# Optimization experiments

Hardware: AMD Instinct MI355X
Metric: run time of the kernel (lower is better)

The kernel has to match this reference:

```python
import jax, jax.numpy as jnp
import numpy as np

B, S, T = 2, 4096, 4096
SRC, DST, WIDTH = 512, 512, 128
BLK = 128  # JAKAL_ADDITIVE_ROUTE_BLOCK_SIZE default


def setup_inputs() -> dict:
    key = jax.random.key(0)
    ks = jax.random.split(key, 7)
    return {
        "source_val": jax.random.normal(ks[0], (B, S, SRC), jnp.float32),
        "target_val": jax.random.normal(ks[1], (B, T, DST), jnp.float32),
        "Ws": jax.random.normal(ks[2], (WIDTH, SRC), jnp.float32) * 0.02,  # source_proj weight
        "Wt": jax.random.normal(ks[3], (WIDTH, DST), jnp.float32) * 0.02,  # target_proj weight
        "ws_out": jax.random.normal(ks[4], (WIDTH,), jnp.float32) * 0.02,  # source_out weight
        "wt_out": jax.random.normal(ks[5], (WIDTH,), jnp.float32) * 0.02,  # target_out weight
        "w_int": jax.random.normal(ks[6], (WIDTH,), jnp.float32) * 0.02,   # interaction_weight
        "bias": jnp.zeros((), jnp.float32),
    }


def reference(source_val, target_val, Ws, Wt, ws_out, wt_out, w_int, bias):
    # Projections (Linear without bias): y = x @ W.T
    ps = jnp.einsum('bsd,wd->bsw', source_val, Ws)   # [B,S,WIDTH]
    pt = jnp.einsum('btd,wd->btw', target_val, Wt)   # [B,T,WIDTH]
    s_lin = jnp.einsum('bsw,w->bs', ps, ws_out)      # [B,S]
    t_lin = jnp.einsum('btw,w->bt', pt, wt_out)      # [B,T]

    nblk = S // BLK
    # Block the source axis, matching the torch block loop (avoids a [B,S,T,W] tensor).
    ps_blocks = ps.reshape(B, nblk, BLK, WIDTH).transpose(1, 0, 2, 3)   # [nblk,B,BLK,W]
    sl_blocks = s_lin.reshape(B, nblk, BLK).transpose(1, 0, 2)          # [nblk,B,BLK]

    def block_scores(_, xs):
        ps_blk, sl_blk = xs
        # SiLU of the elementwise bilinear interaction, then low-rank weighted reduce.
        inter = jax.nn.silu(ps_blk[:, :, None, :] * pt[:, None, :, :])  # [B,BLK,T,W]
        sc = jnp.einsum('bktw,w->bkt', inter, w_int)
        sc = sc + sl_blk[:, :, None] + t_lin[:, None, :] + bias
        return None, sc

    _, out = jax.lax.scan(block_scores, None, (ps_blocks, sl_blocks))   # [nblk,B,BLK,T]
    return out.transpose(1, 0, 2, 3).reshape(B, S, T)
```

## Files before the change

kernel.cpp:

```cpp
#include <hip/hip_runtime.h>
#include <cstdint>
#include <cstddef>

#define B_ 2
#define S_ 4096
#define T_ 4096
#define D_ 512
#define W_ 128

#define A0C (-0.0006958f)
#define A1C (0.2529946f)
#define A2C (-0.0226345f)
#define A3C (0.0022173f)
#define A4C (-0.00011668f)
#define ZCUT 2.5f
#define ROWCAP 65536

typedef __attribute__((ext_vector_type(8))) short bf16x8;
typedef __attribute__((ext_vector_type(4))) float f32x4;

__device__ __forceinline__ uint16_t f2bf(float f){
  uint32_t u = __float_as_uint(f);
  u += 0x7FFFu + ((u >> 16) & 1u);
  return (uint16_t)(u >> 16);
}
__device__ __forceinline__ float bf2f(uint16_t h){
  return __uint_as_float(((uint32_t)h) << 16);
}

__device__ __forceinline__ void gl_lds16(const void* g, void* l){
  __builtin_amdgcn_global_load_lds(
      (const __attribute__((address_space(1))) void*)g,
      (__attribute__((address_space(3))) void*)l, 16, 0, 0);
}

union F4 { float4 v; float f[4]; };

template<int INBF>
__global__ void prep_k(const void* __restrict__ Ws, const void* __restrict__ Wt,
                       const void* __restrict__ wso, const void* __restrict__ wto,
                       const void* __restrict__ wi, const void* __restrict__ bias,
                       float* __restrict__ WsT, float* __restrict__ WtT,
                       float* __restrict__ wsof, float* __restrict__ wtof,
                       float* __restrict__ wif, float* __restrict__ cbias,
                       int* __restrict__ rowCnt){
  auto cv = [](const void* p, int i)->float{
    if (INBF) return bf2f(((const uint16_t*)p)[i]);
    return ((const float*)p)[i];
  };
  const void* in = (blockIdx.x & 1) ? Wt : Ws;
  float* out = (blockIdx.x & 1) ? WtT : WsT;
  int base = (blockIdx.x >> 1) * 4096;
  for (int o = base + threadIdx.x; o < base + 4096; o += blockDim.x){
    int d = o >> 7, w = o & (W_ - 1);
    out[o] = cv(in, w * D_ + d);
  }
  if (blockIdx.x == 0){
    if (threadIdx.x < W_){
      wsof[threadIdx.x] = cv(wso, threadIdx.x);
      wtof[threadIdx.x] = cv(wto, threadIdx.x);
      wif[threadIdx.x]  = cv(wi,  threadIdx.x);
    }
    __syncthreads();
    if (threadIdx.x == 0){
      float s = 0.f;
      for (int k = 0; k < W_; ++k) s += wif[k];
      cbias[0] = cv(bias, 0) + A0C * s;
      rowCnt[0] = 0;
    }
  }
}

template<int INBF, int MODE>
__global__ __launch_bounds__(256) void proj_k(const void* __restrict__ xraw,
        const float* __restrict__ WT, const float* __restrict__ wout,
        const float* __restrict__ wint,
        float* __restrict__ pT, float* __restrict__ lin,
        uint16_t* __restrict__ feat){
  __shared__ float xl[64 * 36];
  __shared__ float wl[64 * 128];
  int tid = threadIdx.x;
  int tx = tid & 31, ty = tid >> 5;
  int rowBase = blockIdx.x * 32;
  float acc[4][4] = {};
  for (int c = 0; c < 8; ++c){
    int d0 = c * 64;
    const float4* wt4 = (const float4*)(WT + (size_t)d0 * W_);
    float4* wl4 = (float4*)wl;
    #pragma unroll
    for (int p = 0; p < 8; ++p){ int q = tid + 256 * p; wl4[q] = wt4[q]; }
    #pragma unroll
    for (int p = 0; p < 2; ++p){
      int q = tid + 256 * p;
      int r = q >> 4, dq = q & 15;
      float v0, v1, v2, v3;
      if (INBF){
        const uint16_t* xp = (const uint16_t*)xraw + (size_t)(rowBase + r) * D_ + d0 + dq * 4;
        ushort4 u = *(const ushort4*)xp;
        v0 = bf2f(u.x); v1 = bf2f(u.y); v2 = bf2f(u.z); v3 = bf2f(u.w);
      } else {
        const float* xp = (const float*)xraw + (size_t)(rowBase + r) * D_ + d0 + dq * 4;
        float4 u = *(const float4*)xp;
        v0 = u.x; v1 = u.y; v2 = u.z; v3 = u.w;
      }
      xl[(dq*4+0)*36 + r] = v0;
      xl[(dq*4+1)*36 + r] = v1;
      xl[(dq*4+2)*36 + r] = v2;
      xl[(dq*4+3)*36 + r] = v3;
    }
    __syncthreads();
    #pragma unroll 4
    for (int d = 0; d < 64; ++d){
      F4 a, w;
      a.v = *(const float4*)(xl + d * 36 + ty * 4);
      w.v = *(const float4*)(wl + d * 128 + tx * 4);
      #pragma unroll
      for (int i = 0; i < 4; ++i)
        #pragma unroll
        for (int j = 0; j < 4; ++j)
          acc[i][j] = fmaf(a.f[i], w.f[j], acc[i][j]);
    }
    __syncthreads();
  }
  float* tile = wl;
  #pragma unroll
  for (int i = 0; i < 4; ++i)
    #pragma unroll
    for (int j = 0; j < 4; ++j)
      tile[(tx*4 + j) * 33 + ty*4 + i] = acc[i][j];
  F4 wo; wo.v = *(const float4*)(wout + tx * 4);
  F4 wiv;
  if (MODE == 0) wiv.v = *(const float4*)(wint + tx * 4);
  #pragma unroll
  for (int i = 0; i < 4; ++i){
    int r = rowBase + ty * 4 + i;
    float s = acc[i][0]*wo.f[0] + acc[i][1]*wo.f[1] + acc[i][2]*wo.f[2] + acc[i][3]*wo.f[3];
    #pragma unroll
    for (int off = 16; off >= 1; off >>= 1) s += __shfl_xor(s, off, 32);
    if (tx == 0) lin[r] = s;
    ushort4 g[5];
    uint16_t* gp = (uint16_t*)g;
    #pragma unroll
    for (int j = 0; j < 4; ++j){
      float p = acc[i][j];
      float p2 = p*p, p4 = p2*p2, p6 = p4*p2, p8 = p4*p4;
      float e0, e1, e2, e3, e4;
      if (MODE == 0){
        float wq = wiv.f[j];
        e0 = 0.5f * wq * p; e1 = A1C * wq * p2; e2 = A2C * wq * p4;
        e3 = A3C * wq * p6; e4 = A4C * wq * p8;
      } else {
        e0 = p; e1 = p2; e2 = p4; e3 = p6; e4 = p8;
      }
      gp[0*4+j] = f2bf(e0); gp[1*4+j] = f2bf(e1); gp[2*4+j] = f2bf(e2);
      gp[3*4+j] = f2bf(e3); gp[4*4+j] = f2bf(e4);
    }
    uint16_t* o = feat + (size_t)r * 640 + tx * 4;
    *(ushort4*)(o)       = g[0];
    *(ushort4*)(o + 128) = g[1];
    *(ushort4*)(o + 256) = g[2];
    *(ushort4*)(o + 384) = g[3];
    *(ushort4*)(o + 512) = g[4];
  }
  __syncthreads();
  {
    int w = tid >> 1, h = tid & 1;
    int b = rowBase >> 12;
    int sb = rowBase & (S_ - 1);
    float* dst = pT + ((size_t)(b * W_ + w)) * S_ + sb + h * 16;
    const float* src = tile + w * 33 + h * 16;
    #pragma unroll
    for (int k = 0; k < 4; ++k){
      float4 o = make_float4(src[k*4+0], src[k*4+1], src[k*4+2], src[k*4+3]);
      *(float4*)(dst + k * 4) = o;
    }
  }
}

__global__ void maxT_k(const float* __restrict__ ptT, float* __restrict__ maxT){
  int bw = blockIdx.x;
  int tid = threadIdx.x;
  const float* c = ptT + (size_t)bw * T_;
  float m = 0.f;
  for (int t = tid; t < T_; t += 256) m = fmaxf(m, fabsf(c[t]));
  #pragma unroll
  for (int off = 32; off >= 1; off >>= 1) m = fmaxf(m, __shfl_xor(m, off, 64));
  __shared__ float red[4];
  if ((tid & 63) == 0) red[tid >> 6] = m;
  __syncthreads();
  if (tid == 0)
    maxT[bw] = fmaxf(fmaxf(red[0], red[1]), fmaxf(red[2], red[3]));
}

template<int OUTBF>
__global__ __launch_bounds__(256) void gemm_k(const uint16_t* __restrict__ fA,
      const uint16_t* __restrict__ fB, const float* __restrict__ slin,
      const float* __restrict__ tlin, const float* __restrict__ cbias,
      void* __restrict__ outv){
  __shared__ __align__(16) uint16_t As[2][128 * 32];
  __shared__ __align__(16) uint16_t Bs[2][128 * 32];
  int tid = threadIdx.x, lane = tid & 63, wv = tid >> 6;
  int quad = lane >> 4, lr = lane & 15;
  int rowT = blockIdx.y * 128, colT = blockIdx.x * 128;
  int b = rowT >> 12;
  int r0 = lane >> 2, c0 = (lane & 3) * 8;
  int mBase = (wv & 1) * 64, nBase = (wv >> 1) * 64;

  f32x4 acc[4][4];
  #pragma unroll
  for (int i = 0; i < 4; ++i)
    #pragma unroll
    for (int j = 0; j < 4; ++j)
      acc[i][j] = (f32x4){0.f, 0.f, 0.f, 0.f};

  const uint16_t* aBase = fA + (size_t)rowT * 640;
  const uint16_t* bBase = fB + ((size_t)b * T_ + colT) * 640;

  const int NSTEP = 20;
  #pragma unroll
  for (int h = 0; h < 2; ++h){
    int q = 2 * wv + h;
    gl_lds16(aBase + (size_t)(16 * q + r0) * 640 + c0, &As[0][q * 512]);
    gl_lds16(bBase + (size_t)(16 * q + r0) * 640 + c0, &Bs[0][q * 512]);
  }
  for (int step = 0; step < NSTEP; ++step){
    int cur = step & 1;
    if (step + 1 < NSTEP){
      int kc = (step + 1) * 32;
      #pragma unroll
      for (int h = 0; h < 2; ++h){
        int q = 2 * wv + h;
        gl_lds16(aBase + (size_t)(16 * q + r0) * 640 + kc + c0, &As[cur ^ 1][q * 512]);
        gl_lds16(bBase + (size_t)(16 * q + r0) * 640 + kc + c0, &Bs[cur ^ 1][q * 512]);
      }
      asm volatile("s_waitcnt vmcnt(4)" ::: "memory");
    } else {
      asm volatile("s_waitcnt vmcnt(0)" ::: "memory");
    }
    __builtin_amdgcn_s_barrier();
    bf16x8 af[4], bfr[4];
    #pragma unroll
    for (int i = 0; i < 4; ++i)
      af[i] = *(const bf16x8*)&As[cur][(mBase + i * 16 + lr) * 32 + quad * 8];
    #pragma unroll
    for (int j = 0; j < 4; ++j)
      bfr[j] = *(const bf16x8*)&Bs[cur][(nBase + j * 16 + lr) * 32 + quad * 8];
    #pragma unroll
    for (int i = 0; i < 4; ++i)
      #pragma unroll
      for (int j = 0; j < 4; ++j)
        acc[i][j] = __builtin_amdgcn_mfma_f32_16x16x32_bf16(bfr[j], af[i], acc[i][j], 0, 0, 0);
    __builtin_amdgcn_s_barrier();
  }

  float cb = cbias[0];
  #pragma unroll
  for (int i = 0; i < 4; ++i){
    int srow = rowT + mBase + i * 16 + lr;
    float sl = slin[srow] + cb;
    #pragma unroll
    for (int j = 0; j < 4; ++j){
      int t0 = colT + nBase + j * 16 + quad * 4;
      F4 tl; tl.v = *(const float4*)(tlin + b * T_ + t0);
      float o0 = acc[i][j][0] + sl + tl.f[0];
      float o1 = acc[i][j][1] + sl + tl.f[1];
      float o2 = acc[i][j][2] + sl + tl.f[2];
      float o3 = acc[i][j][3] + sl + tl.f[3];
      size_t oi = (size_t)srow * T_ + t0;
      if (OUTBF){
        ushort4 pk = make_ushort4(f2bf(o0), f2bf(o1), f2bf(o2), f2bf(o3));
        *(ushort4*)((uint16_t*)outv + oi) = pk;
      } else {
        *(float4*)((float*)outv + oi) = make_float4(o0, o1, o2, o3);
      }
    }
  }
}

__global__ void flagrows_k(const float* __restrict__ psT, const float* __restrict__ maxT,
                           uint32_t* __restrict__ rowList, int* __restrict__ rowCnt){
  int w = blockIdx.x, b = blockIdx.y;
  int tid = threadIdx.x;
  float mt = maxT[b * W_ + w];
  const float* psc = psT + (size_t)(b * W_ + w) * S_;
  for (int s = tid; s < S_; s += 256){
    float p = psc[s];
    if (fabsf(p) * mt > ZCUT){
      int k = atomicAdd(rowCnt, 1);
      if (k < ROWCAP)
        rowList[k] = ((uint32_t)b << 19) | ((uint32_t)w << 12) | (uint32_t)s;
    }
  }
}

template<int OUTBF>
__global__ __launch_bounds__(256) void fixscan_k(const float* __restrict__ psT,
        const float* __restrict__ ptT, const float* __restrict__ wint,
        const uint16_t* __restrict__ fA, const uint16_t* __restrict__ fB,
        const uint32_t* __restrict__ rowList, const int* __restrict__ rowCnt,
        void* __restrict__ outv){
  int n = *rowCnt; if (n > ROWCAP) n = ROWCAP;
  int tid = threadIdx.x;
  for (int job = blockIdx.x; job < n; job += gridDim.x){
    uint32_t pk = rowList[job];
    int b = (int)(pk >> 19), w = (int)((pk >> 12) & 127u), s = (int)(pk & 4095u);
    float wi = wint[w];
    float p = psT[(size_t)(b * W_ + w) * S_ + s];
    const float* ptc = ptT + (size_t)(b * W_ + w) * T_;
    const uint16_t* fa = fA + ((size_t)b * S_ + s) * 640 + w;
    float a0 = bf2f(fa[0]),   a1 = bf2f(fa[128]), a2 = bf2f(fa[256]);
    float a3 = bf2f(fa[384]), a4 = bf2f(fa[512]);
    for (int t = tid; t < T_; t += 256){
      float q = ptc[t];
      float z = p * q;
      if (fabsf(z) > ZCUT){
        const uint16_t* fb = fB + ((size_t)b * T_ + t) * 640 + w;
        float dot = a0 * bf2f(fb[0]) + a1 * bf2f(fb[128]) + a2 * bf2f(fb[256])
                  + a3 * bf2f(fb[384]) + a4 * bf2f(fb[512]);
        float sil = z / (1.0f + __expf(-z));
        float corr = wi * sil - dot - A0C * wi;
        size_t idx = ((size_t)b * S_ + s) * T_ + t;
        if (OUTBF){
          uint32_t* wp = (uint32_t*)outv + (idx >> 1);
          bool hi = (idx & 1u) != 0;
          uint32_t assumed, old = *wp;
          do {
            assumed = old;
            uint16_t h = hi ? (uint16_t)(assumed >> 16) : (uint16_t)(assumed & 0xFFFFu);
            uint16_t nh = f2bf(bf2f(h) + corr);
            uint32_t nw = hi ? ((assumed & 0x0000FFFFu) | ((uint32_t)nh << 16))
                             : ((assumed & 0xFFFF0000u) | (uint32_t)nh);
            old = atomicCAS(wp, assumed, nw);
          } while (old != assumed);
        } else {
          atomicAdd((float*)outv + idx, corr);
        }
      }
    }
  }
}

extern "C" void kernel_launch(void* const* d_in, const int* in_sizes, int n_in,
                              void* d_out, int out_size, void* d_ws, size_t ws_size,
                              hipStream_t stream){
  char* ws = (char*)d_ws;
  size_t off = 0;
  auto alloc = [&](size_t bytes)->char*{
    char* p = ws + off; off += (bytes + 255) & ~(size_t)255; return p;
  };
  float*    WsT  = (float*)   alloc((size_t)D_*W_*4);
  float*    WtT  = (float*)   alloc((size_t)D_*W_*4);
  float*    wsof = (float*)   alloc(W_*4);
  float*    wtof = (float*)   alloc(W_*4);
  float*    wif  = (float*)   alloc(W_*4);
  float*    cbias= (float*)   alloc(4);
  int*      rowCnt=(int*)     alloc(4);
  uint32_t* rowList=(uint32_t*)alloc((size_t)ROWCAP*4);
  float*    psT  = (float*)   alloc((size_t)B_*S_*W_*4);
  float*    ptT  = (float*)   alloc((size_t)B_*T_*W_*4);
  float*    slin = (float*)   alloc((size_t)B_*S_*4);
  float*    tlin = (float*)   alloc((size_t)B_*T_*4);
  float*    maxT = (float*)   alloc((size_t)B_*W_*4);
  uint16_t* featA= (uint16_t*)alloc((size_t)B_*S_*640*2);
  uint16_t* featB= (uint16_t*)alloc((size_t)B_*T_*640*2);

  bool inbf  = (in_sizes[0] == (int)((size_t)B_*S_*D_*2));
  bool outbf = (out_size    == (int)((size_t)B_*S_*T_*2));

  if (inbf){
    hipLaunchKernelGGL((prep_k<1>), dim3(32), dim3(256), 0, stream,
        d_in[2], d_in[3], d_in[4], d_in[5], d_in[6], d_in[7],
        WsT, WtT, wsof, wtof, wif, cbias, rowCnt);
    hipLaunchKernelGGL((proj_k<1,0>), dim3(B_*S_/32), dim3(256), 0, stream,
        d_in[0], WsT, wsof, wif, psT, slin, featA);
    hipLaunchKernelGGL((proj_k<1,1>), dim3(B_*T_/32), dim3(256), 0, stream,
        d_in[1], WtT, wtof, wif, ptT, tlin, featB);
  } else {
    hipLaunchKernelGGL((prep_k<0>), dim3(32), dim3(256), 0, stream,
        d_in[2], d_in[3], d_in[4], d_in[5], d_in[6], d_in[7],
        WsT, WtT, wsof, wtof, wif, cbias, rowCnt);
    hipLaunchKernelGGL((proj_k<0,0>), dim3(B_*S_/32), dim3(256), 0, stream,
        d_in[0], WsT, wsof, wif, psT, slin, featA);
    hipLaunchKernelGGL((proj_k<0,1>), dim3(B_*T_/32), dim3(256), 0, stream,
        d_in[1], WtT, wtof, wif, ptT, tlin, featB);
  }
  hipLaunchKernelGGL(maxT_k, dim3(B_*W_), dim3(256), 0, stream, ptT, maxT);
  if (outbf)
    hipLaunchKernelGGL((gemm_k<1>), dim3(T_/128, B_*S_/128), dim3(256), 0, stream,
        featA, featB, slin, tlin, cbias, d_out);
  else
    hipLaunchKernelGGL((gemm_k<0>), dim3(T_/128, B_*S_/128), dim3(256), 0, stream,
        featA, featB, slin, tlin, cbias, d_out);
  hipLaunchKernelGGL(flagrows_k, dim3(W_, B_), dim3(256), 0, stream,
      psT, maxT, rowList, rowCnt);
  if (outbf)
    hipLaunchKernelGGL((fixscan_k<1>), dim3(2048), dim3(256), 0, stream,
        psT, ptT, wif, featA, featB, rowList, rowCnt, d_out);
  else
    hipLaunchKernelGGL((fixscan_k<0>), dim3(2048), dim3(256), 0, stream,
        psT, ptT, wif, featA, featB, rowList, rowCnt, d_out);
}
```

Before: 314.9 us.

## Fuse maxT into projection and flag-list into fixup kernel, halve proj tile

Removes the standalone maxT reduction kernel: the target projection now folds per-column absolute maxima into maxT through atomicMax on the float bit pattern, and prep_k zeroes maxT. The row-flagging and fixup kernels are merged into one kernel per (w,b) that builds its flagged-row list in shared memory, which removes a launch, the global row counter and the ROWCAP limit. The projection tile shrinks from 32 to 16 rows per block to double the block count, at the cost of reloading the weight slab more times overall. The merged fixup runs only 256 blocks and processes its rows serially per block, so load imbalance across columns may be worse than the old 2048-block job pool.

```diff
diff --git a/kernel.cpp b/kernel.cpp
--- a/kernel.cpp
+++ b/kernel.cpp
@@ -14,7 +14,6 @@
 #define A3C (0.0022173f)
 #define A4C (-0.00011668f)
 #define ZCUT 2.5f
-#define ROWCAP 65536
 
 typedef __attribute__((ext_vector_type(8))) short bf16x8;
 typedef __attribute__((ext_vector_type(4))) float f32x4;
@@ -43,7 +42,7 @@
                        float* __restrict__ WsT, float* __restrict__ WtT,
                        float* __restrict__ wsof, float* __restrict__ wtof,
                        float* __restrict__ wif, float* __restrict__ cbias,
-                       int* __restrict__ rowCnt){
+                       float* __restrict__ maxT){
   auto cv = [](const void* p, int i)->float{
     if (INBF) return bf2f(((const uint16_t*)p)[i]);
     return ((const float*)p)[i];
@@ -55,6 +54,9 @@
     int d = o >> 7, w = o & (W_ - 1);
     out[o] = cv(in, w * D_ + d);
   }
+  if (blockIdx.x == 1){
+    maxT[threadIdx.x] = 0.f;
+  }
   if (blockIdx.x == 0){
     if (threadIdx.x < W_){
       wsof[threadIdx.x] = cv(wso, threadIdx.x);
@@ -66,7 +68,6 @@
       float s = 0.f;
       for (int k = 0; k < W_; ++k) s += wif[k];
       cbias[0] = cv(bias, 0) + A0C * s;
-      rowCnt[0] = 0;
     }
   }
 }
@@ -76,22 +77,21 @@
         const float* __restrict__ WT, const float* __restrict__ wout,
         const float* __restrict__ wint,
         float* __restrict__ pT, float* __restrict__ lin,
-        uint16_t* __restrict__ feat){
-  __shared__ float xl[64 * 36];
+        uint16_t* __restrict__ feat, float* __restrict__ maxT){
+  __shared__ float xl[64 * 18];
   __shared__ float wl[64 * 128];
   int tid = threadIdx.x;
   int tx = tid & 31, ty = tid >> 5;
-  int rowBase = blockIdx.x * 32;
-  float acc[4][4] = {};
+  int rowBase = blockIdx.x * 16;
+  float acc[2][4] = {};
   for (int c = 0; c < 8; ++c){
     int d0 = c * 64;
     const float4* wt4 = (const float4*)(WT + (size_t)d0 * W_);
     float4* wl4 = (float4*)wl;
     #pragma unroll
     for (int p = 0; p < 8; ++p){ int q = tid + 256 * p; wl4[q] = wt4[q]; }
-    #pragma unroll
-    for (int p = 0; p < 2; ++p){
-      int q = tid + 256 * p;
+    {
+      int q = tid;
       int r = q >> 4, dq = q & 15;
       float v0, v1, v2, v3;
       if (INBF){
@@ -103,37 +103,38 @@
         float4 u = *(const float4*)xp;
         v0 = u.x; v1 = u.y; v2 = u.z; v3 = u.w;
       }
-      xl[(dq*4+0)*36 + r] = v0;
-      xl[(dq*4+1)*36 + r] = v1;
-      xl[(dq*4+2)*36 + r] = v2;
-      xl[(dq*4+3)*36 + r] = v3;
+      xl[(dq*4+0)*18 + r] = v0;
+      xl[(dq*4+1)*18 + r] = v1;
+      xl[(dq*4+2)*18 + r] = v2;
+      xl[(dq*4+3)*18 + r] = v3;
     }
     __syncthreads();
     #pragma unroll 4
     for (int d = 0; d < 64; ++d){
-      F4 a, w;
-      a.v = *(const float4*)(xl + d * 36 + ty * 4);
+      float a0 = xl[d * 18 + ty * 2 + 0];
+      float a1 = xl[d * 18 + ty * 2 + 1];
+      F4 w;
       w.v = *(const float4*)(wl + d * 128 + tx * 4);
       #pragma unroll
-      for (int i = 0; i < 4; ++i)
-        #pragma unroll
-        for (int j = 0; j < 4; ++j)
-          acc[i][j] = fmaf(a.f[i], w.f[j], acc[i][j]);
+      for (int j = 0; j < 4; ++j){
+        acc[0][j] = fmaf(a0, w.f[j], acc[0][j]);
+        acc[1][j] = fmaf(a1, w.f[j], acc[1][j]);
+      }
     }
     __syncthreads();
   }
   float* tile = wl;
   #pragma unroll
-  for (int i = 0; i < 4; ++i)
+  for (int i = 0; i < 2; ++i)
     #pragma unroll
     for (int j = 0; j < 4; ++j)
-      tile[(tx*4 + j) * 33 + ty*4 + i] = acc[i][j];
+      tile[(tx*4 + j) * 17 + ty*2 + i] = acc[i][j];
   F4 wo; wo.v = *(const float4*)(wout + tx * 4);
   F4 wiv;
   if (MODE == 0) wiv.v = *(const float4*)(wint + tx * 4);
   #pragma unroll
-  for (int i = 0; i < 4; ++i){
-    int r = rowBase + ty * 4 + i;
+  for (int i = 0; i < 2; ++i){
+    int r = rowBase + ty * 2 + i;
     float s = acc[i][0]*wo.f[0] + acc[i][1]*wo.f[1] + acc[i][2]*wo.f[2] + acc[i][3]*wo.f[3];
     #pragma unroll
     for (int off = 16; off >= 1; off >>= 1) s += __shfl_xor(s, off, 32);
@@ -163,33 +164,25 @@
     *(ushort4*)(o + 512) = g[4];
   }
   __syncthreads();
+  int b = rowBase >> 12;
   {
     int w = tid >> 1, h = tid & 1;
-    int b = rowBase >> 12;
     int sb = rowBase & (S_ - 1);
-    float* dst = pT + ((size_t)(b * W_ + w)) * S_ + sb + h * 16;
-    const float* src = tile + w * 33 + h * 16;
-    #pragma unroll
-    for (int k = 0; k < 4; ++k){
+    float* dst = pT + ((size_t)(b * W_ + w)) * S_ + sb + h * 8;
+    const float* src = tile + w * 17 + h * 8;
+    #pragma unroll
+    for (int k = 0; k < 2; ++k){
       float4 o = make_float4(src[k*4+0], src[k*4+1], src[k*4+2], src[k*4+3]);
       *(float4*)(dst + k * 4) = o;
     }
   }
-}
-
-__global__ void maxT_k(const float* __restrict__ ptT, float* __restrict__ maxT){
-  int bw = blockIdx.x;
-  int tid = threadIdx.x;
-  const float* c = ptT + (size_t)bw * T_;
-  float m = 0.f;
-  for (int t = tid; t < T_; t += 256) m = fmaxf(m, fabsf(c[t]));
-  #pragma unroll
-  for (int off = 32; off >= 1; off >>= 1) m = fmaxf(m, __shfl_xor(m, off, 64));
-  __shared__ float red[4];
-  if ((tid & 63) == 0) red[tid >> 6] = m;
-  __syncthreads();
-  if (tid == 0)
-    maxT[bw] = fmaxf(fmaxf(red[0], red[1]), fmaxf(red[2], red[3]));
+  if (MODE == 1 && tid < W_){
+    int w = tid;
+    float m = 0.f;
+    #pragma unroll
+    for (int r = 0; r < 16; ++r) m = fmaxf(m, fabsf(tile[w * 17 + r]));
+    atomicMax((unsigned int*)&maxT[b * W_ + w], __float_as_uint(m));
+  }
 }
 
 template<int OUTBF>
@@ -277,36 +270,33 @@
   }
 }
 
-__global__ void flagrows_k(const float* __restrict__ psT, const float* __restrict__ maxT,
-                           uint32_t* __restrict__ rowList, int* __restrict__ rowCnt){
+template<int OUTBF>
+__global__ __launch_bounds__(256) void flagfix_k(const float* __restrict__ psT,
+        const float* __restrict__ ptT, const float* __restrict__ wint,
+        const uint16_t* __restrict__ fA, const uint16_t* __restrict__ fB,
+        const float* __restrict__ maxT, void* __restrict__ outv){
+  __shared__ int cnt;
+  __shared__ uint16_t list[S_];
   int w = blockIdx.x, b = blockIdx.y;
   int tid = threadIdx.x;
+  if (tid == 0) cnt = 0;
+  __syncthreads();
   float mt = maxT[b * W_ + w];
   const float* psc = psT + (size_t)(b * W_ + w) * S_;
   for (int s = tid; s < S_; s += 256){
+    if (fabsf(psc[s]) * mt > ZCUT){
+      int k = atomicAdd(&cnt, 1);
+      list[k] = (uint16_t)s;
+    }
+  }
+  __syncthreads();
+  int n = cnt;
+  if (n == 0) return;
+  float wi = wint[w];
+  const float* ptc = ptT + (size_t)(b * W_ + w) * T_;
+  for (int ji = 0; ji < n; ++ji){
+    int s = (int)list[ji];
     float p = psc[s];
-    if (fabsf(p) * mt > ZCUT){
-      int k = atomicAdd(rowCnt, 1);
-      if (k < ROWCAP)
-        rowList[k] = ((uint32_t)b << 19) | ((uint32_t)w << 12) | (uint32_t)s;
-    }
-  }
-}
-
-template<int OUTBF>
-__global__ __launch_bounds__(256) void fixscan_k(const float* __restrict__ psT,
-        const float* __restrict__ ptT, const float* __restrict__ wint,
-        const uint16_t* __restrict__ fA, const uint16_t* __restrict__ fB,
-        const uint32_t* __restrict__ rowList, const int* __restrict__ rowCnt,
-        void* __restrict__ outv){
-  int n = *rowCnt; if (n > ROWCAP) n = ROWCAP;
-  int tid = threadIdx.x;
-  for (int job = blockIdx.x; job < n; job += gridDim.x){
-    uint32_t pk = rowList[job];
-    int b = (int)(pk >> 19), w = (int)((pk >> 12) & 127u), s = (int)(pk & 4095u);
-    float wi = wint[w];
-    float p = psT[(size_t)(b * W_ + w) * S_ + s];
-    const float* ptc = ptT + (size_t)(b * W_ + w) * T_;
     const uint16_t* fa = fA + ((size_t)b * S_ + s) * 640 + w;
     float a0 = bf2f(fa[0]),   a1 = bf2f(fa[128]), a2 = bf2f(fa[256]);
     float a3 = bf2f(fa[384]), a4 = bf2f(fa[512]);
@@ -354,8 +344,6 @@
   float*    wtof = (float*)   alloc(W_*4);
   float*    wif  = (float*)   alloc(W_*4);
   float*    cbias= (float*)   alloc(4);
-  int*      rowCnt=(int*)     alloc(4);
-  uint32_t* rowList=(uint32_t*)alloc((size_t)ROWCAP*4);
   float*    psT  = (float*)   alloc((size_t)B_*S_*W_*4);
   float*    ptT  = (float*)   alloc((size_t)B_*T_*W_*4);
   float*    slin = (float*)   alloc((size_t)B_*S_*4);
@@ -370,33 +358,30 @@
   if (inbf){
     hipLaunchKernelGGL((prep_k<1>), dim3(32), dim3(256), 0, stream,
         d_in[2], d_in[3], d_in[4], d_in[5], d_in[6], d_in[7],
-        WsT, WtT, wsof, wtof, wif, cbias, rowCnt);
-    hipLaunchKernelGGL((proj_k<1,0>), dim3(B_*S_/32), dim3(256), 0, stream,
-        d_in[0], WsT, wsof, wif, psT, slin, featA);
-    hipLaunchKernelGGL((proj_k<1,1>), dim3(B_*T_/32), dim3(256), 0, stream,
-        d_in[1], WtT, wtof, wif, ptT, tlin, featB);
+        WsT, WtT, wsof, wtof, wif, cbias, maxT);
+    hipLaunchKernelGGL((proj_k<1,0>), dim3(B_*S_/16), dim3(256), 0, stream,
+        d_in[0], WsT, wsof, wif, psT, slin, featA, maxT);
+    hipLaunchKernelGGL((proj_k<1,1>), dim3(B_*T_/16), dim3(256), 0, stream,
+        d_in[1], WtT, wtof, wif, ptT, tlin, featB, maxT);
   } else {
     hipLaunchKernelGGL((prep_k<0>), dim3(32), dim3(256), 0, stream,
         d_in[2], d_in[3], d_in[4], d_in[5], d_in[6], d_in[7],
-        WsT, WtT, wsof, wtof, wif, cbias, rowCnt);
-    hipLaunchKernelGGL((proj_k<0,0>), dim3(B_*S_/32), dim3(256), 0, stream,
-        d_in[0], WsT, wsof, wif, psT, slin, featA);
-    hipLaunchKernelGGL((proj_k<0,1>), dim3(B_*T_/32), dim3(256), 0, stream,
-        d_in[1], WtT, wtof, wif, ptT, tlin, featB);
-  }
-  hipLaunchKernelGGL(maxT_k, dim3(B_*W_), dim3(256), 0, stream, ptT, maxT);
+        WsT, WtT, wsof, wtof, wif, cbias, maxT);
+    hipLaunchKernelGGL((proj_k<0,0>), dim3(B_*S_/16), dim3(256), 0, stream,
+        d_in[0], WsT, wsof, wif, psT, slin, featA, maxT);
+    hipLaunchKernelGGL((proj_k<0,1>), dim3(B_*T_/16), dim3(256), 0, stream,
+        d_in[1], WtT, wtof, wif, ptT, tlin, featB, maxT);
+  }
   if (outbf)
     hipLaunchKernelGGL((gemm_k<1>), dim3(T_/128, B_*S_/128), dim3(256), 0, stream,
         featA, featB, slin, tlin, cbias, d_out);
   else
     hipLaunchKernelGGL((gemm_k<0>), dim3(T_/128, B_*S_/128), dim3(256), 0, stream,
         featA, featB, slin, tlin, cbias, d_out);
-  hipLaunchKernelGGL(flagrows_k, dim3(W_, B_), dim3(256), 0, stream,
-      psT, maxT, rowList, rowCnt);
   if (outbf)
-    hipLaunchKernelGGL((fixscan_k<1>), dim3(2048), dim3(256), 0, stream,
-        psT, ptT, wif, featA, featB, rowList, rowCnt, d_out);
+    hipLaunchKernelGGL((flagfix_k<1>), dim3(W_, B_), dim3(256), 0, stream,
+        psT, ptT, wif, featA, featB, maxT, d_out);
   else
-    hipLaunchKernelGGL((fixscan_k<0>), dim3(2048), dim3(256), 0, stream,
-        psT, ptT, wif, featA, featB, rowList, rowCnt, d_out);
-}
+    hipLaunchKernelGGL((flagfix_k<0>), dim3(W_, B_), dim3(256), 0, stream,
+        psT, ptT, wif, featA, featB, maxT, d_out);
+}
```

New measurement: 508.5 us. 1.61x slower.
